# Kernel optimization log

Hardware: AMD Instinct MI355X
Metric: run time of the kernel (lower is better)

The kernel has to match this reference:

```python
import jax, jax.numpy as jnp
import numpy as np

N = 100000   # nodes
E = 1600000  # edges (avg degree 16)
D = 30       # in channels
H = 4        # attention heads
C = 30       # per-head out channels
EPS = 1e-5
NEG_SLOPE = 0.2


def setup_inputs() -> dict:
    ks = jax.random.split(jax.random.key(0), 12)
    s = 0.1
    return {
        "h": jax.random.normal(ks[0], (N, D), jnp.float32),
        "edge_index": jax.random.randint(ks[1], (2, E), 0, N),
        "edge_weight": jax.random.uniform(ks[2], (E,), jnp.float32),
        "bn_gamma": jnp.ones((D,), jnp.float32),
        "bn_beta": jnp.zeros((D,), jnp.float32),
        "W": jax.random.normal(ks[3], (D, H * C), jnp.float32) * s,
        "att_src": jax.random.normal(ks[4], (H, C), jnp.float32) * s,
        "att_dst": jax.random.normal(ks[5], (H, C), jnp.float32) * s,
        "att_edge": jax.random.normal(ks[6], (H, C), jnp.float32) * s,
        "W_edge": jax.random.normal(ks[7], (1, H * C), jnp.float32) * s,
        "bias": jnp.zeros((C,), jnp.float32),
        "fc1_w": jax.random.normal(ks[8], (C, C), jnp.float32) * s,
        "fc1_b": jnp.zeros((C,), jnp.float32),
        "fc2_w": jax.random.normal(ks[9], (C, C), jnp.float32) * s,
        "fc2_b": jnp.zeros((C,), jnp.float32),
        "fc3_w": jax.random.normal(ks[10], (C, C), jnp.float32) * s,
        "fc3_b": jnp.zeros((C,), jnp.float32),
    }


def reference(h, edge_index, edge_weight, bn_gamma, bn_beta, W, att_src, att_dst,
              att_edge, W_edge, bias, fc1_w, fc1_b, fc2_w, fc2_b, fc3_w, fc3_b):
    n = h.shape[0]
    # BatchNorm1d, training-mode batch statistics (biased variance)
    mu = h.mean(0)
    var = ((h - mu) ** 2).mean(0)
    hn = (h - mu) * jax.lax.rsqrt(var + EPS) * bn_gamma + bn_beta

    # GATConv with add_self_loops=True; self-loop edge_attr = mean edge weight
    # (PyG fill_value='mean' default)
    loop = jnp.arange(n)
    src = jnp.concatenate([edge_index[0], loop])
    dst = jnp.concatenate([edge_index[1], loop])
    ew = jnp.concatenate([edge_weight, jnp.full((n,), edge_weight.mean(), h.dtype)])

    x = (hn @ W).reshape(n, H, C)                    # [N,H,C] shared src/dst lin
    a_src = (x * att_src).sum(-1)                    # [N,H]
    a_dst = (x * att_dst).sum(-1)                    # [N,H]
    e = (ew[:, None] * W_edge[0]).reshape(-1, H, C)  # [E2,H,C] lin_edge (no bias)
    a_edge = (e * att_edge).sum(-1)                  # [E2,H]

    alpha = jax.nn.leaky_relu(a_src[src] + a_dst[dst] + a_edge, NEG_SLOPE)
    # scatter-softmax over incoming edges of each destination node
    m = jax.ops.segment_max(alpha, dst, num_segments=n)
    ex = jnp.exp(alpha - m[dst])
    den = jax.ops.segment_sum(ex, dst, num_segments=n)
    alpha = ex / (den[dst] + 1e-16)                  # [E2,H]

    out = jax.ops.segment_sum(x[src] * alpha[:, :, None], dst, num_segments=n)
    out = out.mean(1) + bias                         # concat=False -> head mean

    out = jax.nn.relu(out)
    out = jax.nn.relu(out @ fc1_w.T + fc1_b)
    out = jax.nn.relu(out @ fc2_w.T + fc2_b)
    return out @ fc3_w.T + fc3_b
```

## Files before the change

kernel.cpp:

```cpp
#include <hip/hip_runtime.h>
#include <hip/hip_fp16.h>

#define N_NODES 100000
#define N_EDGES 1600000
#define D_IN 30
#define H_HEADS 4
#define C_OUT 30
#define EPSV 1e-5f
#define NEG 0.2f
#define MAXDEG 48
#define NPB 64
#define NBUCK 256
#define BUCK_NODES 391
#define BUCK_CAP 7000
#define EPB 2048
#define BIN_BLOCKS ((N_EDGES + EPB - 1) / EPB)
#define STATS_BLOCKS 448
#define X_BLOCKS ((N_NODES + NPB - 1) / NPB)
#define NODE_BLOCKS ((N_NODES + 63) / 64)

#define OFF_XH    0
#define OFF_ADST  6400000
#define OFF_PAR   6800000
#define OFF_DEG   6804096
#define OFF_STATS 6904256
#define OFF_GCUR  6904320
#define OFF_ADJ   6908416
#define OFF_GBUF  11708416

__device__ __forceinline__ float hb2f(unsigned int bits) {
    __half_raw r; r.x = (unsigned short)bits;
    return __half2float(*reinterpret_cast<__half*>(&r));
}

__global__ __launch_bounds__(256) void k_bin(const int* __restrict__ ei,
                                             const float* __restrict__ ew,
                                             const float* __restrict__ h,
                                             int* __restrict__ gcur,
                                             uint2* __restrict__ gbuf,
                                             float* __restrict__ stats) {
    int t = threadIdx.x;
    if (blockIdx.x < BIN_BLOCKS) {
        __shared__ int bcnt[NBUCK];
        __shared__ int basel[NBUCK];
        bcnt[t] = 0;
        __syncthreads();
        int j0 = blockIdx.x * EPB + t;
        unsigned lo_[8]; int d_[8], b_[8], r_[8];
#pragma unroll
        for (int r = 0; r < 8; ++r) {
            int j = j0 + r * 256;
            d_[r] = -1;
            if (j < N_EDGES) {
                int s = ei[j];
                int d = ei[N_EDGES + j];
                float w = ew[j];
                __half hv = __float2half_rn(w);
                unsigned short hb = *reinterpret_cast<unsigned short*>(&hv);
                lo_[r] = ((unsigned)s << 15) | (unsigned)(hb & 0x7FFFu);
                d_[r] = d;
                b_[r] = d / BUCK_NODES;
                r_[r] = atomicAdd(&bcnt[b_[r]], 1);
            }
        }
        __syncthreads();
        { int c = bcnt[t]; basel[t] = c ? atomicAdd(&gcur[t * 16], c) : 0; }
        __syncthreads();
#pragma unroll
        for (int r = 0; r < 8; ++r) {
            if (d_[r] >= 0) {
                int gi = basel[b_[r]] + r_[r];
                if (gi < BUCK_CAP)
                    gbuf[(size_t)b_[r] * BUCK_CAP + gi] = make_uint2(lo_[r], (unsigned)d_[r]);
            }
        }
        return;
    }
    __shared__ float ls[61];
    if (t < 61) ls[t] = 0.f;
    __syncthreads();
    float s[D_IN], q[D_IN];
#pragma unroll
    for (int d = 0; d < D_IN; ++d) { s[d] = 0.f; q[d] = 0.f; }
    int idx0 = (blockIdx.x - BIN_BLOCKS) * 256 + t;
    int stride = STATS_BLOCKS * 256;
    for (int r = idx0; r < N_NODES; r += stride) {
        const float* row = h + r * D_IN;
#pragma unroll
        for (int d = 0; d < D_IN; ++d) { float v = row[d]; s[d] += v; q[d] += v * v; }
    }
    float es = 0.f;
    for (int i = idx0; i < N_EDGES; i += stride) es += ew[i];
#pragma unroll
    for (int d = 0; d < D_IN; ++d) {
        for (int off = 32; off; off >>= 1) {
            s[d] += __shfl_down(s[d], off);
            q[d] += __shfl_down(q[d], off);
        }
    }
    for (int off = 32; off; off >>= 1) es += __shfl_down(es, off);
    if ((t & 63) == 0) {
#pragma unroll
        for (int d = 0; d < D_IN; ++d) { atomicAdd(&ls[d], s[d]); atomicAdd(&ls[30 + d], q[d]); }
        atomicAdd(&ls[60], es);
    }
    __syncthreads();
    if (t < 61) atomicAdd(&stats[t], ls[t]);
}

__global__ __launch_bounds__(256) void k_bx(const int* __restrict__ gcur,
                                            const uint2* __restrict__ gbuf,
                                            unsigned int* __restrict__ adj,
                                            int* __restrict__ deg,
                                            const float* __restrict__ h,
                                            const float* __restrict__ W,
                                            const float* __restrict__ Wedge,
                                            const float* __restrict__ att_edge,
                                            const float* __restrict__ att_src,
                                            const float* __restrict__ att_dst,
                                            const float* __restrict__ gamma,
                                            const float* __restrict__ beta,
                                            const float* __restrict__ stats,
                                            float* __restrict__ par,
                                            unsigned int* __restrict__ xh,
                                            float* __restrict__ adst) {
    __shared__ __align__(16) unsigned char smem[38416];
    int t = threadIdx.x;
    if (blockIdx.x < 2 * NBUCK) {
        unsigned* rows = (unsigned*)smem;
        int* cnt = (int*)(smem + 37632);
        int bb = blockIdx.x;
        int b = bb >> 1, half = bb & 1;
        int lo = b * BUCK_NODES + half * 196;
        int span = half ? (BUCK_NODES - 196) : 196;
        int lim = N_NODES - lo; if (lim > span) lim = span; if (lim < 0) lim = 0;
        for (int i = t; i < 196; i += 256) cnt[i] = 0;
        __syncthreads();
        int cb = gcur[b * 16]; if (cb > BUCK_CAP) cb = BUCK_CAP;
        for (int r = t; r < cb; r += 256) {
            uint2 rec = gbuf[(size_t)b * BUCK_CAP + r];
            int li = (int)rec.y - lo;
            if (li >= 0 && li < lim) {
                int p = atomicAdd(&cnt[li], 1);
                if (p < MAXDEG) rows[li * MAXDEG + p] = rec.x;
            }
        }
        __syncthreads();
        int tot = lim * MAXDEG;
        for (int i = t; i < tot; i += 256) {
            int li = i / MAXDEG;
            int p = i - li * MAXDEG;
            if (p < cnt[li]) adj[(size_t)lo * MAXDEG + i] = rows[i];
        }
        for (int i = t; i < lim; i += 256) { int c = cnt[i]; deg[lo + i] = (c > MAXDEG) ? MAXDEG : c; }
        return;
    }
    float* W2s = (float*)smem;
    float* hs  = (float*)(smem + 14400);
    float* psd = (float*)(smem + 22080);
    float* cq  = (float*)(smem + 23040);
    float* b2s = (float*)(smem + 23072);
    float* scs = (float*)(smem + 23552);
    float* shs = (float*)(smem + 23672);
    int bx = blockIdx.x - 2 * NBUCK;
    if (t < D_IN) {
        float mu = stats[t] * (1.f / N_NODES);
        float var = stats[30 + t] * (1.f / N_NODES) - mu * mu;
        float inv = 1.f / sqrtf(var + EPSV);
        float sc = gamma[t] * inv;
        scs[t] = sc; shs[t] = beta[t] - mu * sc;
    }
    __syncthreads();
    for (int i = t; i < 3600; i += 256) W2s[i] = scs[i / 120] * W[i];
    if (t >= 128 && t < 248) {
        int c = t - 128;
        float b = 0.f;
#pragma unroll
        for (int d = 0; d < D_IN; ++d) b = fmaf(shs[d], W[d * 120 + c], b);
        b2s[c] = b;
    }
    if (bx == 0 && t >= 248 && t < 252) {
        int hh = t - 248;
        float k = 0.f;
        for (int c = 0; c < 30; ++c) k = fmaf(Wedge[hh * 30 + c], att_edge[hh * 30 + c], k);
        par[64 + hh] = k;
    }
    if (bx == 0 && t == 252) par[68] = stats[60] * (1.f / N_EDGES);
    __syncthreads();
    int base = bx * NPB;
    int cnt2 = N_NODES - base; if (cnt2 > NPB) cnt2 = NPB;
    if (t < 240) {
        int d = t >> 3, q = t & 7, hh = q & 3;
        const float* att = (q < 4) ? att_src : att_dst;
        float sum = 0.f;
#pragma unroll
        for (int c = 0; c < 30; ++c) sum = fmaf(W2s[d * 120 + hh * 30 + c], att[hh * 30 + c], sum);
        psd[t] = sum;
    }
    if (t >= 240 && t < 248) {
        int q = t - 240, hh = q & 3;
        const float* att = (q < 4) ? att_src : att_dst;
        float sum = 0.f;
#pragma unroll
        for (int c = 0; c < 30; ++c) sum = fmaf(b2s[hh * 30 + c], att[hh * 30 + c], sum);
        cq[q] = sum;
    }
    for (int i = t; i < cnt2 * 30; i += 256) hs[i] = h[(size_t)base * 30 + i];
    __syncthreads();
    const float2* W2p = (const float2*)W2s;
    int total = cnt2 * 60;
    for (int o = t; o < total; o += 256) {
        int node = o / 60, p = o - node * 60;
        const float* hrow = hs + node * 30;
        float ax = b2s[2 * p], ay = b2s[2 * p + 1];
        const float2* Wp = W2p + p;
#pragma unroll
        for (int d = 0; d < 30; ++d) {
            float hv = hrow[d];
            float2 w = Wp[d * 60];
            ax = fmaf(hv, w.x, ax);
            ay = fmaf(hv, w.y, ay);
        }
        __half2 pk = __float22half2_rn(make_float2(ax, ay));
        int hh = p / 15, j = p - hh * 15;
        xh[(size_t)(base + node) * 64 + hh * 16 + j] = *reinterpret_cast<unsigned int*>(&pk);
    }
    for (int v = t; v < cnt2 * 8; v += 256) {
        int node = v >> 3, q = v & 7;
        const float* hrow = hs + node * 30;
        float sum = cq[q];
#pragma unroll
        for (int d = 0; d < 30; ++d) sum = fmaf(hrow[d], psd[d * 8 + q], sum);
        int n = base + node;
        if (q < 4) xh[(size_t)n * 64 + q * 16 + 15] = __float_as_uint(sum);
        else       adst[n * H_HEADS + (q - 4)] = sum;
    }
}

__global__ __launch_bounds__(256) void k_node(const uint4* __restrict__ xh4,
                                              const float* __restrict__ adst,
                                              const float* __restrict__ par,
                                              const int* __restrict__ deg,
                                              const unsigned int* __restrict__ adj,
                                              const float* __restrict__ bias,
                                              const float* __restrict__ fc1w,
                                              const float* __restrict__ fc1b,
                                              const float* __restrict__ fc2w,
                                              const float* __restrict__ fc2b,
                                              const float* __restrict__ fc3w,
                                              const float* __restrict__ fc3b,
                                              float* __restrict__ out) {
    __shared__ float Ws[3][900];
    __shared__ float Bs[3][30];
    __shared__ float bias_s[32];
    __shared__ float tb[64 * 32];
    int t = threadIdx.x;
    for (int i = t; i < 900; i += 256) { Ws[0][i] = fc1w[i]; Ws[1][i] = fc2w[i]; Ws[2][i] = fc3w[i]; }
    if (t < 30) { Bs[0][t] = fc1b[t]; Bs[1][t] = fc2b[t]; Bs[2][t] = fc3b[t]; }
    if (t < 32) bias_s[t] = (t < 30) ? bias[t] : 0.f;
    __syncthreads();

    int l = t & 63;
    int k = l & 15;
    int wv = t >> 6;
    int q = (l >> 4) & 3;
    int h = k >> 2;
    int asl_b = (((l & 48) | (k & 12) | 3) << 2);
    int pb4 = (l & 48) << 2;
    float kh = par[64 + h];
    float ew_mean = par[68];
    int ch = (k & 3) * 8;

    for (int g = 0; g < 4; ++g) {
        int nl = g * 16 + wv * 4 + q;
        int n = blockIdx.x * 64 + nl;
        bool vn = (n < N_NODES);
        unsigned nn = vn ? (unsigned)n : 0u;
        float adn = adst[nn * H_HEADS + h];
        int dn = vn ? min(deg[nn], MAXDEG) : 0;
        int dmax = dn;
        dmax = max(dmax, __shfl_xor(dmax, 16));
        dmax = max(dmax, __shfl_xor(dmax, 32));

        const unsigned int* arow = adj + (size_t)nn * MAXDEG;
        unsigned int aw0 = arow[k];
        unsigned int aw1 = 0, aw2 = 0;
        if (dmax > 16) aw1 = arow[16 + k];
        if (dmax > 32) aw2 = arow[32 + k];

        uint4 rw = xh4[nn * 16u + (unsigned)k];
        float asn = __uint_as_float((unsigned)__builtin_amdgcn_ds_bpermute(asl_b, (int)rw.w));
        float z = fmaf(ew_mean, kh, adn) + asn;
        z = fmaxf(z, NEG * z);
        float e0 = __expf(z);
        float den = e0;
        float2 x0 = __half22float2(*(const __half2*)&rw.x);
        float2 x1 = __half22float2(*(const __half2*)&rw.y);
        float2 x2 = __half22float2(*(const __half2*)&rw.z);
        float2 x3 = __half22float2(*(const __half2*)&rw.w);
        float2 a0 = make_float2(e0 * x0.x, e0 * x0.y);
        float2 a1 = make_float2(e0 * x1.x, e0 * x1.y);
        float2 a2 = make_float2(e0 * x2.x, e0 * x2.y);
        float2 a3 = make_float2(e0 * x3.x, e0 * x3.y);

#pragma unroll 2
        for (int u = 0; u < dmax; ++u) {
            unsigned int aw = (u < 16) ? aw0 : ((u < 32) ? aw1 : aw2);
            unsigned int ewd = (unsigned)__builtin_amdgcn_ds_bpermute(pb4 + ((u & 15) << 2), (int)aw);
            bool valid = (u < dn);
            unsigned s = valid ? (ewd >> 15) : nn;
            uint4 r = xh4[s * 16u + (unsigned)k];
            float w = hb2f(ewd & 0x7FFFu);
            float as_ = __uint_as_float((unsigned)__builtin_amdgcn_ds_bpermute(asl_b, (int)r.w));
            float zz = fmaf(w, kh, adn) + as_;
            zz = fmaxf(zz, NEG * zz);
            float ee = __expf(zz);
            ee = valid ? ee : 0.f;
            den += ee;
            float2 y0 = __half22float2(*(const __half2*)&r.x);
            float2 y1 = __half22float2(*(const __half2*)&r.y);
            float2 y2 = __half22float2(*(const __half2*)&r.z);
            float2 y3 = __half22float2(*(const __half2*)&r.w);
            a0.x = fmaf(ee, y0.x, a0.x); a0.y = fmaf(ee, y0.y, a0.y);
            a1.x = fmaf(ee, y1.x, a1.x); a1.y = fmaf(ee, y1.y, a1.y);
            a2.x = fmaf(ee, y2.x, a2.x); a2.y = fmaf(ee, y2.y, a2.y);
            a3.x = fmaf(ee, y3.x, a3.x); a3.y = fmaf(ee, y3.y, a3.y);
        }

        float rden = 0.25f / (den + 1e-16f);
        a0.x *= rden; a0.y *= rden; a1.x *= rden; a1.y *= rden;
        a2.x *= rden; a2.y *= rden; a3.x *= rden; a3.y *= rden;

        a0.x += __shfl_xor(a0.x, 4); a0.y += __shfl_xor(a0.y, 4);
        a1.x += __shfl_xor(a1.x, 4); a1.y += __shfl_xor(a1.y, 4);
        a2.x += __shfl_xor(a2.x, 4); a2.y += __shfl_xor(a2.y, 4);
        a3.x += __shfl_xor(a3.x, 4); a3.y += __shfl_xor(a3.y, 4);
        a0.x += __shfl_xor(a0.x, 8); a0.y += __shfl_xor(a0.y, 8);
        a1.x += __shfl_xor(a1.x, 8); a1.y += __shfl_xor(a1.y, 8);
        a2.x += __shfl_xor(a2.x, 8); a2.y += __shfl_xor(a2.y, 8);
        a3.x += __shfl_xor(a3.x, 8); a3.y += __shfl_xor(a3.y, 8);

        if (vn && (k & 12) == 0) {
            float v0 = fmaxf(a0.x + bias_s[ch + 0], 0.f);
            float v1 = fmaxf(a0.y + bias_s[ch + 1], 0.f);
            float v2 = fmaxf(a1.x + bias_s[ch + 2], 0.f);
            float v3 = fmaxf(a1.y + bias_s[ch + 3], 0.f);
            float v4 = fmaxf(a2.x + bias_s[ch + 4], 0.f);
            float v5 = fmaxf(a2.y + bias_s[ch + 5], 0.f);
            float v6 = fmaxf(a3.x + bias_s[ch + 6], 0.f);
            float v7 = fmaxf(a3.y + bias_s[ch + 7], 0.f);
            float* p = tb + nl * 32 + ch;
            *(float4*)p       = make_float4(v0, v1, v2, v3);
            *(float4*)(p + 4) = make_float4(v4, v5, v6, v7);
        }
    }
    __syncthreads();

    int base = blockIdx.x * 64;
    for (int lay = 0; lay < 3; ++lay) {
        float y[8];
#pragma unroll
        for (int j = 0; j < 8; ++j) {
            int i = t + j * 256;
            int nd = i >> 5, c = i & 31;
            y[j] = 0.f;
            if (c < 30 && base + nd < N_NODES) {
                float acc = Bs[lay][c];
                const float* Wl = &Ws[lay][c * 30];
                const float* tr = &tb[nd * 32];
#pragma unroll
                for (int cc = 0; cc < 30; ++cc) acc = fmaf(tr[cc], Wl[cc], acc);
                y[j] = (lay < 2) ? fmaxf(acc, 0.f) : acc;
            }
        }
        __syncthreads();
#pragma unroll
        for (int j = 0; j < 8; ++j) {
            int i = t + j * 256;
            int nd = i >> 5, c = i & 31;
            if (c < 30 && base + nd < N_NODES) {
                if (lay < 2) tb[nd * 32 + c] = y[j];
                else out[(size_t)(base + nd) * 30 + c] = y[j];
            }
        }
        if (lay < 2) __syncthreads();
    }
}

extern "C" void kernel_launch(void* const* d_in, const int* in_sizes, int n_in,
                              void* d_out, int out_size, void* d_ws, size_t ws_size,
                              hipStream_t stream) {
    const float* h        = (const float*)d_in[0];
    const int*   ei       = (const int*)d_in[1];
    const float* ew       = (const float*)d_in[2];
    const float* gamma    = (const float*)d_in[3];
    const float* beta     = (const float*)d_in[4];
    const float* W        = (const float*)d_in[5];
    const float* att_src  = (const float*)d_in[6];
    const float* att_dst  = (const float*)d_in[7];
    const float* att_edge = (const float*)d_in[8];
    const float* Wedge    = (const float*)d_in[9];
    const float* bias     = (const float*)d_in[10];
    const float* fc1w     = (const float*)d_in[11];
    const float* fc1b     = (const float*)d_in[12];
    const float* fc2w     = (const float*)d_in[13];
    const float* fc2b     = (const float*)d_in[14];
    const float* fc3w     = (const float*)d_in[15];
    const float* fc3b     = (const float*)d_in[16];

    float*        ws    = (float*)d_ws;
    unsigned int* xh    = (unsigned int*)(ws + OFF_XH);
    float*        adstb = ws + OFF_ADST;
    float*        par   = ws + OFF_PAR;
    float*        stats = ws + OFF_STATS;
    int*          deg   = (int*)(ws + OFF_DEG);
    int*          gcur  = (int*)(ws + OFF_GCUR);
    unsigned int* adj   = (unsigned int*)(ws + OFF_ADJ);
    uint2*        gbuf  = (uint2*)(ws + OFF_GBUF);
    float*        out   = (float*)d_out;

    hipMemsetAsync(stats, 0, (64 + NBUCK * 16) * 4, stream);

    k_bin<<<BIN_BLOCKS + STATS_BLOCKS, 256, 0, stream>>>(ei, ew, h, gcur, gbuf, stats);
    k_bx<<<2 * NBUCK + X_BLOCKS, 256, 0, stream>>>(gcur, gbuf, adj, deg, h, W, Wedge,
                                                   att_edge, att_src, att_dst,
                                                   gamma, beta, stats, par, xh, adstb);
    k_node<<<NODE_BLOCKS, 256, 0, stream>>>((const uint4*)xh, adstb, par, deg, adj,
                                            bias, fc1w, fc1b, fc2w, fc2b, fc3w, fc3b, out);
}
```

Before: 198.4 us.

## Compute MLP in registers via shuffles and shrink node blocks to 16 nodes

k_node now handles 16 nodes per block, one per 16-lane group, instead of looping over 64 nodes per block. The three 30x30 layers are computed in registers with cross-lane shuffles against transposed weights in shared memory, which removes the shared tile buffer and the block barriers between layers. This raises block count and parallelism but repeats the weight load into shared memory in four times as many blocks. Separately, k_bin moves to 512-thread blocks that each cover twice as many edges, with half as many stats blocks.

```diff
diff --git a/kernel.cpp b/kernel.cpp
--- a/kernel.cpp
+++ b/kernel.cpp
@@ -13,11 +13,11 @@
 #define NBUCK 256
 #define BUCK_NODES 391
 #define BUCK_CAP 7000
-#define EPB 2048
+#define EPB 4096
 #define BIN_BLOCKS ((N_EDGES + EPB - 1) / EPB)
-#define STATS_BLOCKS 448
+#define STATS_BLOCKS 224
 #define X_BLOCKS ((N_NODES + NPB - 1) / NPB)
-#define NODE_BLOCKS ((N_NODES + 63) / 64)
+#define NODE_BLOCKS (N_NODES / 16)
 
 #define OFF_XH    0
 #define OFF_ADST  6400000
@@ -33,7 +33,7 @@
     return __half2float(*reinterpret_cast<__half*>(&r));
 }
 
-__global__ __launch_bounds__(256) void k_bin(const int* __restrict__ ei,
+__global__ __launch_bounds__(512) void k_bin(const int* __restrict__ ei,
                                              const float* __restrict__ ew,
                                              const float* __restrict__ h,
                                              int* __restrict__ gcur,
@@ -43,13 +43,13 @@
     if (blockIdx.x < BIN_BLOCKS) {
         __shared__ int bcnt[NBUCK];
         __shared__ int basel[NBUCK];
-        bcnt[t] = 0;
+        if (t < NBUCK) bcnt[t] = 0;
         __syncthreads();
         int j0 = blockIdx.x * EPB + t;
         unsigned lo_[8]; int d_[8], b_[8], r_[8];
 #pragma unroll
         for (int r = 0; r < 8; ++r) {
-            int j = j0 + r * 256;
+            int j = j0 + r * 512;
             d_[r] = -1;
             if (j < N_EDGES) {
                 int s = ei[j];
@@ -64,7 +64,7 @@
             }
         }
         __syncthreads();
-        { int c = bcnt[t]; basel[t] = c ? atomicAdd(&gcur[t * 16], c) : 0; }
+        if (t < NBUCK) { int c = bcnt[t]; basel[t] = c ? atomicAdd(&gcur[t * 16], c) : 0; }
         __syncthreads();
 #pragma unroll
         for (int r = 0; r < 8; ++r) {
@@ -82,8 +82,8 @@
     float s[D_IN], q[D_IN];
 #pragma unroll
     for (int d = 0; d < D_IN; ++d) { s[d] = 0.f; q[d] = 0.f; }
-    int idx0 = (blockIdx.x - BIN_BLOCKS) * 256 + t;
-    int stride = STATS_BLOCKS * 256;
+    int idx0 = (blockIdx.x - BIN_BLOCKS) * 512 + t;
+    int stride = STATS_BLOCKS * 512;
     for (int r = idx0; r < N_NODES; r += stride) {
         const float* row = h + r * D_IN;
 #pragma unroll
@@ -250,13 +250,31 @@
                                               const float* __restrict__ fc3w,
                                               const float* __restrict__ fc3b,
                                               float* __restrict__ out) {
-    __shared__ float Ws[3][900];
-    __shared__ float Bs[3][30];
+    __shared__ float WsT[3][960];
+    __shared__ float BsT[3][32];
     __shared__ float bias_s[32];
-    __shared__ float tb[64 * 32];
     int t = threadIdx.x;
-    for (int i = t; i < 900; i += 256) { Ws[0][i] = fc1w[i]; Ws[1][i] = fc2w[i]; Ws[2][i] = fc3w[i]; }
-    if (t < 30) { Bs[0][t] = fc1b[t]; Bs[1][t] = fc2b[t]; Bs[2][t] = fc3b[t]; }
+    {
+        const float4* s0 = (const float4*)fc1w;
+        const float4* s1 = (const float4*)fc2w;
+        const float4* s2 = (const float4*)fc3w;
+        for (int i = t; i < 225; i += 256) {
+            float4 f0 = s0[i], f1 = s1[i], f2 = s2[i];
+            int e = i * 4;
+#pragma unroll
+            for (int u = 0; u < 4; ++u) {
+                int el = e + u, c = el / 30, cc = el - c * 30;
+                float v0 = (u == 0) ? f0.x : (u == 1) ? f0.y : (u == 2) ? f0.z : f0.w;
+                float v1 = (u == 0) ? f1.x : (u == 1) ? f1.y : (u == 2) ? f1.z : f1.w;
+                float v2 = (u == 0) ? f2.x : (u == 1) ? f2.y : (u == 2) ? f2.z : f2.w;
+                WsT[0][cc * 32 + c] = v0;
+                WsT[1][cc * 32 + c] = v1;
+                WsT[2][cc * 32 + c] = v2;
+            }
+        }
+    }
+    if (t < 30) { BsT[0][t] = fc1b[t]; BsT[1][t] = fc2b[t]; BsT[2][t] = fc3b[t]; }
+    if (t >= 30 && t < 32) { BsT[0][t] = 0.f; BsT[1][t] = 0.f; BsT[2][t] = 0.f; }
     if (t < 32) bias_s[t] = (t < 30) ? bias[t] : 0.f;
     __syncthreads();
 
@@ -264,127 +282,113 @@
     int k = l & 15;
     int wv = t >> 6;
     int q = (l >> 4) & 3;
+    int n = blockIdx.x * 16 + wv * 4 + q;
     int h = k >> 2;
     int asl_b = (((l & 48) | (k & 12) | 3) << 2);
     int pb4 = (l & 48) << 2;
+
     float kh = par[64 + h];
     float ew_mean = par[68];
-    int ch = (k & 3) * 8;
-
-    for (int g = 0; g < 4; ++g) {
-        int nl = g * 16 + wv * 4 + q;
-        int n = blockIdx.x * 64 + nl;
-        bool vn = (n < N_NODES);
-        unsigned nn = vn ? (unsigned)n : 0u;
-        float adn = adst[nn * H_HEADS + h];
-        int dn = vn ? min(deg[nn], MAXDEG) : 0;
-        int dmax = dn;
-        dmax = max(dmax, __shfl_xor(dmax, 16));
-        dmax = max(dmax, __shfl_xor(dmax, 32));
-
-        const unsigned int* arow = adj + (size_t)nn * MAXDEG;
-        unsigned int aw0 = arow[k];
-        unsigned int aw1 = 0, aw2 = 0;
-        if (dmax > 16) aw1 = arow[16 + k];
-        if (dmax > 32) aw2 = arow[32 + k];
-
-        uint4 rw = xh4[nn * 16u + (unsigned)k];
-        float asn = __uint_as_float((unsigned)__builtin_amdgcn_ds_bpermute(asl_b, (int)rw.w));
-        float z = fmaf(ew_mean, kh, adn) + asn;
-        z = fmaxf(z, NEG * z);
-        float e0 = __expf(z);
-        float den = e0;
-        float2 x0 = __half22float2(*(const __half2*)&rw.x);
-        float2 x1 = __half22float2(*(const __half2*)&rw.y);
-        float2 x2 = __half22float2(*(const __half2*)&rw.z);
-        float2 x3 = __half22float2(*(const __half2*)&rw.w);
-        float2 a0 = make_float2(e0 * x0.x, e0 * x0.y);
-        float2 a1 = make_float2(e0 * x1.x, e0 * x1.y);
-        float2 a2 = make_float2(e0 * x2.x, e0 * x2.y);
-        float2 a3 = make_float2(e0 * x3.x, e0 * x3.y);
+    float adn = adst[n * H_HEADS + h];
+
+    int dn = min(deg[n], MAXDEG);
+    int dmax = dn;
+    dmax = max(dmax, __shfl_xor(dmax, 16));
+    dmax = max(dmax, __shfl_xor(dmax, 32));
+
+    const unsigned int* arow = adj + (size_t)n * MAXDEG;
+    unsigned int aw0 = arow[k];
+    unsigned int aw1 = 0, aw2 = 0;
+    if (dmax > 16) aw1 = arow[16 + k];
+    if (dmax > 32) aw2 = arow[32 + k];
+
+    uint4 rw = xh4[(unsigned)n * 16u + (unsigned)k];
+    float asn = __uint_as_float((unsigned)__builtin_amdgcn_ds_bpermute(asl_b, (int)rw.w));
+    float z = fmaf(ew_mean, kh, adn) + asn;
+    z = fmaxf(z, NEG * z);
+    float e0 = __expf(z);
+    float den = e0;
+    float2 x0 = __half22float2(*(const __half2*)&rw.x);
+    float2 x1 = __half22float2(*(const __half2*)&rw.y);
+    float2 x2 = __half22float2(*(const __half2*)&rw.z);
+    float2 x3 = __half22float2(*(const __half2*)&rw.w);
+    float2 a0 = make_float2(e0 * x0.x, e0 * x0.y);
+    float2 a1 = make_float2(e0 * x1.x, e0 * x1.y);
+    float2 a2 = make_float2(e0 * x2.x, e0 * x2.y);
+    float2 a3 = make_float2(e0 * x3.x, e0 * x3.y);
 
 #pragma unroll 2
-        for (int u = 0; u < dmax; ++u) {
-            unsigned int aw = (u < 16) ? aw0 : ((u < 32) ? aw1 : aw2);
-            unsigned int ewd = (unsigned)__builtin_amdgcn_ds_bpermute(pb4 + ((u & 15) << 2), (int)aw);
-            bool valid = (u < dn);
-            unsigned s = valid ? (ewd >> 15) : nn;
-            uint4 r = xh4[s * 16u + (unsigned)k];
-            float w = hb2f(ewd & 0x7FFFu);
-            float as_ = __uint_as_float((unsigned)__builtin_amdgcn_ds_bpermute(asl_b, (int)r.w));
-            float zz = fmaf(w, kh, adn) + as_;
-            zz = fmaxf(zz, NEG * zz);
-            float ee = __expf(zz);
-            ee = valid ? ee : 0.f;
-            den += ee;
-            float2 y0 = __half22float2(*(const __half2*)&r.x);
-            float2 y1 = __half22float2(*(const __half2*)&r.y);
-            float2 y2 = __half22float2(*(const __half2*)&r.z);
-            float2 y3 = __half22float2(*(const __half2*)&r.w);
-            a0.x = fmaf(ee, y0.x, a0.x); a0.y = fmaf(ee, y0.y, a0.y);
-            a1.x = fmaf(ee, y1.x, a1.x); a1.y = fmaf(ee, y1.y, a1.y);
-            a2.x = fmaf(ee, y2.x, a2.x); a2.y = fmaf(ee, y2.y, a2.y);
-            a3.x = fmaf(ee, y3.x, a3.x); a3.y = fmaf(ee, y3.y, a3.y);
-        }
-
-        float rden = 0.25f / (den + 1e-16f);
-        a0.x *= rden; a0.y *= rden; a1.x *= rden; a1.y *= rden;
-        a2.x *= rden; a2.y *= rden; a3.x *= rden; a3.y *= rden;
-
-        a0.x += __shfl_xor(a0.x, 4); a0.y += __shfl_xor(a0.y, 4);
-        a1.x += __shfl_xor(a1.x, 4); a1.y += __shfl_xor(a1.y, 4);
-        a2.x += __shfl_xor(a2.x, 4); a2.y += __shfl_xor(a2.y, 4);
-        a3.x += __shfl_xor(a3.x, 4); a3.y += __shfl_xor(a3.y, 4);
-        a0.x += __shfl_xor(a0.x, 8); a0.y += __shfl_xor(a0.y, 8);
-        a1.x += __shfl_xor(a1.x, 8); a1.y += __shfl_xor(a1.y, 8);
-        a2.x += __shfl_xor(a2.x, 8); a2.y += __shfl_xor(a2.y, 8);
-        a3.x += __shfl_xor(a3.x, 8); a3.y += __shfl_xor(a3.y, 8);
-
-        if (vn && (k & 12) == 0) {
-            float v0 = fmaxf(a0.x + bias_s[ch + 0], 0.f);
-            float v1 = fmaxf(a0.y + bias_s[ch + 1], 0.f);
-            float v2 = fmaxf(a1.x + bias_s[ch + 2], 0.f);
-            float v3 = fmaxf(a1.y + bias_s[ch + 3], 0.f);
-            float v4 = fmaxf(a2.x + bias_s[ch + 4], 0.f);
-            float v5 = fmaxf(a2.y + bias_s[ch + 5], 0.f);
-            float v6 = fmaxf(a3.x + bias_s[ch + 6], 0.f);
-            float v7 = fmaxf(a3.y + bias_s[ch + 7], 0.f);
-            float* p = tb + nl * 32 + ch;
-            *(float4*)p       = make_float4(v0, v1, v2, v3);
-            *(float4*)(p + 4) = make_float4(v4, v5, v6, v7);
-        }
-    }
-    __syncthreads();
-
-    int base = blockIdx.x * 64;
-    for (int lay = 0; lay < 3; ++lay) {
-        float y[8];
-#pragma unroll
-        for (int j = 0; j < 8; ++j) {
-            int i = t + j * 256;
-            int nd = i >> 5, c = i & 31;
-            y[j] = 0.f;
-            if (c < 30 && base + nd < N_NODES) {
-                float acc = Bs[lay][c];
-                const float* Wl = &Ws[lay][c * 30];
-                const float* tr = &tb[nd * 32];
-#pragma unroll
-                for (int cc = 0; cc < 30; ++cc) acc = fmaf(tr[cc], Wl[cc], acc);
-                y[j] = (lay < 2) ? fmaxf(acc, 0.f) : acc;
-            }
-        }
-        __syncthreads();
-#pragma unroll
-        for (int j = 0; j < 8; ++j) {
-            int i = t + j * 256;
-            int nd = i >> 5, c = i & 31;
-            if (c < 30 && base + nd < N_NODES) {
-                if (lay < 2) tb[nd * 32 + c] = y[j];
-                else out[(size_t)(base + nd) * 30 + c] = y[j];
-            }
-        }
-        if (lay < 2) __syncthreads();
-    }
+    for (int u = 0; u < dmax; ++u) {
+        unsigned int aw = (u < 16) ? aw0 : ((u < 32) ? aw1 : aw2);
+        unsigned int ewd = (unsigned)__builtin_amdgcn_ds_bpermute(pb4 + ((u & 15) << 2), (int)aw);
+        bool valid = (u < dn);
+        unsigned s = valid ? (ewd >> 15) : (unsigned)n;
+        uint4 r = xh4[s * 16u + (unsigned)k];
+        float w = hb2f(ewd & 0x7FFFu);
+        float as_ = __uint_as_float((unsigned)__builtin_amdgcn_ds_bpermute(asl_b, (int)r.w));
+        float zz = fmaf(w, kh, adn) + as_;
+        zz = fmaxf(zz, NEG * zz);
+        float ee = __expf(zz);
+        ee = valid ? ee : 0.f;
+        den += ee;
+        float2 y0 = __half22float2(*(const __half2*)&r.x);
+        float2 y1 = __half22float2(*(const __half2*)&r.y);
+        float2 y2 = __half22float2(*(const __half2*)&r.z);
+        float2 y3 = __half22float2(*(const __half2*)&r.w);
+        a0.x = fmaf(ee, y0.x, a0.x); a0.y = fmaf(ee, y0.y, a0.y);
+        a1.x = fmaf(ee, y1.x, a1.x); a1.y = fmaf(ee, y1.y, a1.y);
+        a2.x = fmaf(ee, y2.x, a2.x); a2.y = fmaf(ee, y2.y, a2.y);
+        a3.x = fmaf(ee, y3.x, a3.x); a3.y = fmaf(ee, y3.y, a3.y);
+    }
+
+    float rden = 0.25f / (den + 1e-16f);
+    a0.x *= rden; a0.y *= rden; a1.x *= rden; a1.y *= rden;
+    a2.x *= rden; a2.y *= rden; a3.x *= rden; a3.y *= rden;
+
+    a0.x += __shfl_xor(a0.x, 4); a0.y += __shfl_xor(a0.y, 4);
+    a1.x += __shfl_xor(a1.x, 4); a1.y += __shfl_xor(a1.y, 4);
+    a2.x += __shfl_xor(a2.x, 4); a2.y += __shfl_xor(a2.y, 4);
+    a3.x += __shfl_xor(a3.x, 4); a3.y += __shfl_xor(a3.y, 4);
+    a0.x += __shfl_xor(a0.x, 8); a0.y += __shfl_xor(a0.y, 8);
+    a1.x += __shfl_xor(a1.x, 8); a1.y += __shfl_xor(a1.y, 8);
+    a2.x += __shfl_xor(a2.x, 8); a2.y += __shfl_xor(a2.y, 8);
+    a3.x += __shfl_xor(a3.x, 8); a3.y += __shfl_xor(a3.y, 8);
+
+    int kb = (k & 3) * 8;
+    a0.x = fmaxf(a0.x + bias_s[kb + 0], 0.f);
+    a0.y = fmaxf(a0.y + bias_s[kb + 1], 0.f);
+    a1.x = fmaxf(a1.x + bias_s[kb + 2], 0.f);
+    a1.y = fmaxf(a1.y + bias_s[kb + 3], 0.f);
+    a2.x = fmaxf(a2.x + bias_s[kb + 4], 0.f);
+    a2.y = fmaxf(a2.y + bias_s[kb + 5], 0.f);
+    a3.x = fmaxf(a3.x + bias_s[kb + 6], 0.f);
+    a3.y = fmaxf(a3.y + bias_s[kb + 7], 0.f);
+
+    int qb = l & 48;
+    float pr[8] = {a0.x, a0.y, a1.x, a1.y, a2.x, a2.y, a3.x, a3.y};
+    float2 y;
+    y.x = BsT[0][2 * k]; y.y = BsT[0][2 * k + 1];
+#pragma unroll
+    for (int cc = 0; cc < 30; ++cc) {
+        float b = __shfl(pr[cc & 7], qb + (cc >> 3));
+        float2 w2 = *(float2*)&WsT[0][cc * 32 + 2 * k];
+        y.x = fmaf(b, w2.x, y.x); y.y = fmaf(b, w2.y, y.y);
+    }
+    y.x = fmaxf(y.x, 0.f); y.y = fmaxf(y.y, 0.f);
+#pragma unroll
+    for (int lay = 1; lay < 3; ++lay) {
+        float2 y2;
+        y2.x = BsT[lay][2 * k]; y2.y = BsT[lay][2 * k + 1];
+#pragma unroll
+        for (int cc = 0; cc < 30; ++cc) {
+            float b = __shfl((cc & 1) ? y.y : y.x, qb + (cc >> 1));
+            float2 w2 = *(float2*)&WsT[lay][cc * 32 + 2 * k];
+            y2.x = fmaf(b, w2.x, y2.x); y2.y = fmaf(b, w2.y, y2.y);
+        }
+        if (lay < 2) { y2.x = fmaxf(y2.x, 0.f); y2.y = fmaxf(y2.y, 0.f); }
+        y = y2;
+    }
+    if (k < 15) *(float2*)(out + (size_t)n * 30 + 2 * k) = y;
 }
 
 extern "C" void kernel_launch(void* const* d_in, const int* in_sizes, int n_in,
@@ -421,7 +425,7 @@
 
     hipMemsetAsync(stats, 0, (64 + NBUCK * 16) * 4, stream);
 
-    k_bin<<<BIN_BLOCKS + STATS_BLOCKS, 256, 0, stream>>>(ei, ew, h, gcur, gbuf, stats);
+    k_bin<<<BIN_BLOCKS + STATS_BLOCKS, 512, 0, stream>>>(ei, ew, h, gcur, gbuf, stats);
     k_bx<<<2 * NBUCK + X_BLOCKS, 256, 0, stream>>>(gcur, gbuf, adj, deg, h, W, Wedge,
                                                    att_edge, att_src, att_dst,
                                                    gamma, beta, stats, par, xh, adstb);
```

Measured after the change: 197.0 us. No clear change (-0.7%).

## Split attention aggregation from MLP epilogue and enlarge binning blocks

Applied to the files above, without the earlier changes.

The node kernel now handles 16 nodes per block with no shared-memory MLP weights, which gives many more, lighter blocks for the irregular neighbour gather. Its per-node head-averaged results go to a new global scratch buffer. A separate k_out kernel reads that buffer and applies bias, ReLU and the three FC layers, using a shared tile padded to a 31-float row stride to reduce bank conflicts. The edge-binning kernel moves to 512-thread blocks handling 4096 edges each, with half as many stats blocks. The split costs roughly 25 MB of extra global round-trip traffic plus one more kernel launch.

```diff
diff --git a/kernel.cpp b/kernel.cpp
--- a/kernel.cpp
+++ b/kernel.cpp
@@ -13,11 +13,12 @@
 #define NBUCK 256
 #define BUCK_NODES 391
 #define BUCK_CAP 7000
-#define EPB 2048
+#define EPB 4096
 #define BIN_BLOCKS ((N_EDGES + EPB - 1) / EPB)
-#define STATS_BLOCKS 448
+#define STATS_BLOCKS 224
 #define X_BLOCKS ((N_NODES + NPB - 1) / NPB)
-#define NODE_BLOCKS ((N_NODES + 63) / 64)
+#define NODE_BLOCKS (N_NODES / 16)
+#define OUT_BLOCKS ((N_NODES + 63) / 64)
 
 #define OFF_XH    0
 #define OFF_ADST  6400000
@@ -27,13 +28,14 @@
 #define OFF_GCUR  6904320
 #define OFF_ADJ   6908416
 #define OFF_GBUF  11708416
+#define OFF_PRE   15292416
 
 __device__ __forceinline__ float hb2f(unsigned int bits) {
     __half_raw r; r.x = (unsigned short)bits;
     return __half2float(*reinterpret_cast<__half*>(&r));
 }
 
-__global__ __launch_bounds__(256) void k_bin(const int* __restrict__ ei,
+__global__ __launch_bounds__(512) void k_bin(const int* __restrict__ ei,
                                              const float* __restrict__ ew,
                                              const float* __restrict__ h,
                                              int* __restrict__ gcur,
@@ -43,13 +45,13 @@
     if (blockIdx.x < BIN_BLOCKS) {
         __shared__ int bcnt[NBUCK];
         __shared__ int basel[NBUCK];
-        bcnt[t] = 0;
+        if (t < NBUCK) bcnt[t] = 0;
         __syncthreads();
         int j0 = blockIdx.x * EPB + t;
         unsigned lo_[8]; int d_[8], b_[8], r_[8];
 #pragma unroll
         for (int r = 0; r < 8; ++r) {
-            int j = j0 + r * 256;
+            int j = j0 + r * 512;
             d_[r] = -1;
             if (j < N_EDGES) {
                 int s = ei[j];
@@ -64,7 +66,7 @@
             }
         }
         __syncthreads();
-        { int c = bcnt[t]; basel[t] = c ? atomicAdd(&gcur[t * 16], c) : 0; }
+        if (t < NBUCK) { int c = bcnt[t]; basel[t] = c ? atomicAdd(&gcur[t * 16], c) : 0; }
         __syncthreads();
 #pragma unroll
         for (int r = 0; r < 8; ++r) {
@@ -82,8 +84,8 @@
     float s[D_IN], q[D_IN];
 #pragma unroll
     for (int d = 0; d < D_IN; ++d) { s[d] = 0.f; q[d] = 0.f; }
-    int idx0 = (blockIdx.x - BIN_BLOCKS) * 256 + t;
-    int stride = STATS_BLOCKS * 256;
+    int idx0 = (blockIdx.x - BIN_BLOCKS) * 512 + t;
+    int stride = STATS_BLOCKS * 512;
     for (int r = idx0; r < N_NODES; r += stride) {
         const float* row = h + r * D_IN;
 #pragma unroll
@@ -242,121 +244,117 @@
                                               const float* __restrict__ par,
                                               const int* __restrict__ deg,
                                               const unsigned int* __restrict__ adj,
-                                              const float* __restrict__ bias,
-                                              const float* __restrict__ fc1w,
-                                              const float* __restrict__ fc1b,
-                                              const float* __restrict__ fc2w,
-                                              const float* __restrict__ fc2b,
-                                              const float* __restrict__ fc3w,
-                                              const float* __restrict__ fc3b,
-                                              float* __restrict__ out) {
-    __shared__ float Ws[3][900];
-    __shared__ float Bs[3][30];
-    __shared__ float bias_s[32];
-    __shared__ float tb[64 * 32];
+                                              float* __restrict__ pre) {
     int t = threadIdx.x;
-    for (int i = t; i < 900; i += 256) { Ws[0][i] = fc1w[i]; Ws[1][i] = fc2w[i]; Ws[2][i] = fc3w[i]; }
-    if (t < 30) { Bs[0][t] = fc1b[t]; Bs[1][t] = fc2b[t]; Bs[2][t] = fc3b[t]; }
-    if (t < 32) bias_s[t] = (t < 30) ? bias[t] : 0.f;
-    __syncthreads();
-
     int l = t & 63;
     int k = l & 15;
     int wv = t >> 6;
     int q = (l >> 4) & 3;
+    int n = blockIdx.x * 16 + wv * 4 + q;
     int h = k >> 2;
     int asl_b = (((l & 48) | (k & 12) | 3) << 2);
     int pb4 = (l & 48) << 2;
+
     float kh = par[64 + h];
     float ew_mean = par[68];
-    int ch = (k & 3) * 8;
-
-    for (int g = 0; g < 4; ++g) {
-        int nl = g * 16 + wv * 4 + q;
-        int n = blockIdx.x * 64 + nl;
-        bool vn = (n < N_NODES);
-        unsigned nn = vn ? (unsigned)n : 0u;
-        float adn = adst[nn * H_HEADS + h];
-        int dn = vn ? min(deg[nn], MAXDEG) : 0;
-        int dmax = dn;
-        dmax = max(dmax, __shfl_xor(dmax, 16));
-        dmax = max(dmax, __shfl_xor(dmax, 32));
-
-        const unsigned int* arow = adj + (size_t)nn * MAXDEG;
-        unsigned int aw0 = arow[k];
-        unsigned int aw1 = 0, aw2 = 0;
-        if (dmax > 16) aw1 = arow[16 + k];
-        if (dmax > 32) aw2 = arow[32 + k];
-
-        uint4 rw = xh4[nn * 16u + (unsigned)k];
-        float asn = __uint_as_float((unsigned)__builtin_amdgcn_ds_bpermute(asl_b, (int)rw.w));
-        float z = fmaf(ew_mean, kh, adn) + asn;
-        z = fmaxf(z, NEG * z);
-        float e0 = __expf(z);
-        float den = e0;
-        float2 x0 = __half22float2(*(const __half2*)&rw.x);
-        float2 x1 = __half22float2(*(const __half2*)&rw.y);
-        float2 x2 = __half22float2(*(const __half2*)&rw.z);
-        float2 x3 = __half22float2(*(const __half2*)&rw.w);
-        float2 a0 = make_float2(e0 * x0.x, e0 * x0.y);
-        float2 a1 = make_float2(e0 * x1.x, e0 * x1.y);
-        float2 a2 = make_float2(e0 * x2.x, e0 * x2.y);
-        float2 a3 = make_float2(e0 * x3.x, e0 * x3.y);
+    float adn = adst[n * H_HEADS + h];
+
+    int dn = deg[n];
+    dn = min(dn, MAXDEG);
+    int dmax = dn;
+    dmax = max(dmax, __shfl_xor(dmax, 16));
+    dmax = max(dmax, __shfl_xor(dmax, 32));
+
+    const unsigned int* arow = adj + (size_t)n * MAXDEG;
+    unsigned int aw0 = arow[k];
+    unsigned int aw1 = arow[16 + k];
+    unsigned int aw2 = arow[32 + k];
+
+    uint4 rw = xh4[(unsigned)n * 16u + (unsigned)k];
+    float asn = __uint_as_float((unsigned)__builtin_amdgcn_ds_bpermute(asl_b, (int)rw.w));
+    float z = fmaf(ew_mean, kh, adn) + asn;
+    z = fmaxf(z, NEG * z);
+    float e0 = __expf(z);
+    float den = e0;
+    float2 x0 = __half22float2(*(const __half2*)&rw.x);
+    float2 x1 = __half22float2(*(const __half2*)&rw.y);
+    float2 x2 = __half22float2(*(const __half2*)&rw.z);
+    float2 x3 = __half22float2(*(const __half2*)&rw.w);
+    float2 a0 = make_float2(e0 * x0.x, e0 * x0.y);
+    float2 a1 = make_float2(e0 * x1.x, e0 * x1.y);
+    float2 a2 = make_float2(e0 * x2.x, e0 * x2.y);
+    float2 a3 = make_float2(e0 * x3.x, e0 * x3.y);
 
 #pragma unroll 2
-        for (int u = 0; u < dmax; ++u) {
-            unsigned int aw = (u < 16) ? aw0 : ((u < 32) ? aw1 : aw2);
-            unsigned int ewd = (unsigned)__builtin_amdgcn_ds_bpermute(pb4 + ((u & 15) << 2), (int)aw);
-            bool valid = (u < dn);
-            unsigned s = valid ? (ewd >> 15) : nn;
-            uint4 r = xh4[s * 16u + (unsigned)k];
-            float w = hb2f(ewd & 0x7FFFu);
-            float as_ = __uint_as_float((unsigned)__builtin_amdgcn_ds_bpermute(asl_b, (int)r.w));
-            float zz = fmaf(w, kh, adn) + as_;
-            zz = fmaxf(zz, NEG * zz);
-            float ee = __expf(zz);
-            ee = valid ? ee : 0.f;
-            den += ee;
-            float2 y0 = __half22float2(*(const __half2*)&r.x);
-            float2 y1 = __half22float2(*(const __half2*)&r.y);
-            float2 y2 = __half22float2(*(const __half2*)&r.z);
-            float2 y3 = __half22float2(*(const __half2*)&r.w);
-            a0.x = fmaf(ee, y0.x, a0.x); a0.y = fmaf(ee, y0.y, a0.y);
-            a1.x = fmaf(ee, y1.x, a1.x); a1.y = fmaf(ee, y1.y, a1.y);
-            a2.x = fmaf(ee, y2.x, a2.x); a2.y = fmaf(ee, y2.y, a2.y);
-            a3.x = fmaf(ee, y3.x, a3.x); a3.y = fmaf(ee, y3.y, a3.y);
-        }
-
-        float rden = 0.25f / (den + 1e-16f);
-        a0.x *= rden; a0.y *= rden; a1.x *= rden; a1.y *= rden;
-        a2.x *= rden; a2.y *= rden; a3.x *= rden; a3.y *= rden;
-
-        a0.x += __shfl_xor(a0.x, 4); a0.y += __shfl_xor(a0.y, 4);
-        a1.x += __shfl_xor(a1.x, 4); a1.y += __shfl_xor(a1.y, 4);
-        a2.x += __shfl_xor(a2.x, 4); a2.y += __shfl_xor(a2.y, 4);
-        a3.x += __shfl_xor(a3.x, 4); a3.y += __shfl_xor(a3.y, 4);
-        a0.x += __shfl_xor(a0.x, 8); a0.y += __shfl_xor(a0.y, 8);
-        a1.x += __shfl_xor(a1.x, 8); a1.y += __shfl_xor(a1.y, 8);
-        a2.x += __shfl_xor(a2.x, 8); a2.y += __shfl_xor(a2.y, 8);
-        a3.x += __shfl_xor(a3.x, 8); a3.y += __shfl_xor(a3.y, 8);
-
-        if (vn && (k & 12) == 0) {
-            float v0 = fmaxf(a0.x + bias_s[ch + 0], 0.f);
-            float v1 = fmaxf(a0.y + bias_s[ch + 1], 0.f);
-            float v2 = fmaxf(a1.x + bias_s[ch + 2], 0.f);
-            float v3 = fmaxf(a1.y + bias_s[ch + 3], 0.f);
-            float v4 = fmaxf(a2.x + bias_s[ch + 4], 0.f);
-            float v5 = fmaxf(a2.y + bias_s[ch + 5], 0.f);
-            float v6 = fmaxf(a3.x + bias_s[ch + 6], 0.f);
-            float v7 = fmaxf(a3.y + bias_s[ch + 7], 0.f);
-            float* p = tb + nl * 32 + ch;
-            *(float4*)p       = make_float4(v0, v1, v2, v3);
-            *(float4*)(p + 4) = make_float4(v4, v5, v6, v7);
-        }
-    }
-    __syncthreads();
-
+    for (int u = 0; u < dmax; ++u) {
+        unsigned int aw = (u < 16) ? aw0 : ((u < 32) ? aw1 : aw2);
+        unsigned int ewd = (unsigned)__builtin_amdgcn_ds_bpermute(pb4 + ((u & 15) << 2), (int)aw);
+        bool valid = (u < dn);
+        unsigned s = valid ? (ewd >> 15) : (unsigned)n;
+        uint4 r = xh4[s * 16u + (unsigned)k];
+        float w = hb2f(ewd & 0x7FFFu);
+        float as_ = __uint_as_float((unsigned)__builtin_amdgcn_ds_bpermute(asl_b, (int)r.w));
+        float zz = fmaf(w, kh, adn) + as_;
+        zz = fmaxf(zz, NEG * zz);
+        float ee = __expf(zz);
+        ee = valid ? ee : 0.f;
+        den += ee;
+        float2 y0 = __half22float2(*(const __half2*)&r.x);
+        float2 y1 = __half22float2(*(const __half2*)&r.y);
+        float2 y2 = __half22float2(*(const __half2*)&r.z);
+        float2 y3 = __half22float2(*(const __half2*)&r.w);
+        a0.x = fmaf(ee, y0.x, a0.x); a0.y = fmaf(ee, y0.y, a0.y);
+        a1.x = fmaf(ee, y1.x, a1.x); a1.y = fmaf(ee, y1.y, a1.y);
+        a2.x = fmaf(ee, y2.x, a2.x); a2.y = fmaf(ee, y2.y, a2.y);
+        a3.x = fmaf(ee, y3.x, a3.x); a3.y = fmaf(ee, y3.y, a3.y);
+    }
+
+    float rden = 0.25f / (den + 1e-16f);
+    a0.x *= rden; a0.y *= rden; a1.x *= rden; a1.y *= rden;
+    a2.x *= rden; a2.y *= rden; a3.x *= rden; a3.y *= rden;
+
+    a0.x += __shfl_xor(a0.x, 4); a0.y += __shfl_xor(a0.y, 4);
+    a1.x += __shfl_xor(a1.x, 4); a1.y += __shfl_xor(a1.y, 4);
+    a2.x += __shfl_xor(a2.x, 4); a2.y += __shfl_xor(a2.y, 4);
+    a3.x += __shfl_xor(a3.x, 4); a3.y += __shfl_xor(a3.y, 4);
+    a0.x += __shfl_xor(a0.x, 8); a0.y += __shfl_xor(a0.y, 8);
+    a1.x += __shfl_xor(a1.x, 8); a1.y += __shfl_xor(a1.y, 8);
+    a2.x += __shfl_xor(a2.x, 8); a2.y += __shfl_xor(a2.y, 8);
+    a3.x += __shfl_xor(a3.x, 8); a3.y += __shfl_xor(a3.y, 8);
+
+    if ((k & 12) == 0) {
+        float* p = pre + (size_t)n * 32 + k * 8;
+        *(float4*)p       = make_float4(a0.x, a0.y, a1.x, a1.y);
+        *(float4*)(p + 4) = make_float4(a2.x, a2.y, a3.x, a3.y);
+    }
+}
+
+__global__ __launch_bounds__(256) void k_out(const float* __restrict__ pre,
+                                             const float* __restrict__ bias,
+                                             const float* __restrict__ fc1w,
+                                             const float* __restrict__ fc1b,
+                                             const float* __restrict__ fc2w,
+                                             const float* __restrict__ fc2b,
+                                             const float* __restrict__ fc3w,
+                                             const float* __restrict__ fc3b,
+                                             float* __restrict__ out) {
+    __shared__ float Ws[3][900];
+    __shared__ float Bs[3][30];
+    __shared__ float bias_s[30];
+    __shared__ float tb[64 * 31];
+    int t = threadIdx.x;
+    for (int i = t; i < 900; i += 256) { Ws[0][i] = fc1w[i]; Ws[1][i] = fc2w[i]; Ws[2][i] = fc3w[i]; }
+    if (t < 30) { Bs[0][t] = fc1b[t]; Bs[1][t] = fc2b[t]; Bs[2][t] = fc3b[t]; bias_s[t] = bias[t]; }
     int base = blockIdx.x * 64;
+    __syncthreads();
+    for (int i = t; i < 64 * 32; i += 256) {
+        int nd = i >> 5, c = i & 31;
+        if (base + nd < N_NODES && c < 30) {
+            float v = pre[(size_t)base * 32 + i];
+            tb[nd * 31 + c] = fmaxf(v + bias_s[c], 0.f);
+        }
+    }
+    __syncthreads();
     for (int lay = 0; lay < 3; ++lay) {
         float y[8];
 #pragma unroll
@@ -367,7 +365,7 @@
             if (c < 30 && base + nd < N_NODES) {
                 float acc = Bs[lay][c];
                 const float* Wl = &Ws[lay][c * 30];
-                const float* tr = &tb[nd * 32];
+                const float* tr = &tb[nd * 31];
 #pragma unroll
                 for (int cc = 0; cc < 30; ++cc) acc = fmaf(tr[cc], Wl[cc], acc);
                 y[j] = (lay < 2) ? fmaxf(acc, 0.f) : acc;
@@ -379,7 +377,7 @@
             int i = t + j * 256;
             int nd = i >> 5, c = i & 31;
             if (c < 30 && base + nd < N_NODES) {
-                if (lay < 2) tb[nd * 32 + c] = y[j];
+                if (lay < 2) tb[nd * 31 + c] = y[j];
                 else out[(size_t)(base + nd) * 30 + c] = y[j];
             }
         }
@@ -417,14 +415,16 @@
     int*          gcur  = (int*)(ws + OFF_GCUR);
     unsigned int* adj   = (unsigned int*)(ws + OFF_ADJ);
     uint2*        gbuf  = (uint2*)(ws + OFF_GBUF);
+    float*        pre   = ws + OFF_PRE;
     float*        out   = (float*)d_out;
 
     hipMemsetAsync(stats, 0, (64 + NBUCK * 16) * 4, stream);
 
-    k_bin<<<BIN_BLOCKS + STATS_BLOCKS, 256, 0, stream>>>(ei, ew, h, gcur, gbuf, stats);
+    k_bin<<<BIN_BLOCKS + STATS_BLOCKS, 512, 0, stream>>>(ei, ew, h, gcur, gbuf, stats);
     k_bx<<<2 * NBUCK + X_BLOCKS, 256, 0, stream>>>(gcur, gbuf, adj, deg, h, W, Wedge,
                                                    att_edge, att_src, att_dst,
                                                    gamma, beta, stats, par, xh, adstb);
-    k_node<<<NODE_BLOCKS, 256, 0, stream>>>((const uint4*)xh, adstb, par, deg, adj,
-                                            bias, fc1w, fc1b, fc2w, fc2b, fc3w, fc3b, out);
-}
+    k_node<<<NODE_BLOCKS, 256, 0, stream>>>((const uint4*)xh, adstb, par, deg, adj, pre);
+    k_out<<<OUT_BLOCKS, 256, 0, stream>>>(pre, bias, fc1w, fc1b, fc2w, fc2b,
+                                          fc3w, fc3b, out);
+}
```

Result: slower. 214.3 us (+8.0%).
